# Kernel optimization log

Measured on AMD Instinct MI355X. Metric: run time of the kernel, lower is better.

The kernel has to match this reference:

```python
import jax, jax.numpy as jnp
import numpy as np

EMB_DIM = 256
NUM_HEADS = 4
HEAD_DIM = EMB_DIM // NUM_HEADS
N_EDGES = 320000
N_NODES = 10000
EPS = 1e-16  # torch_geometric softmax epsilon


def setup_inputs() -> dict:
    key = jax.random.key(0)
    kq, kk, ki, kw1, kb1, kw2 = jax.random.split(key, 6)
    q = jax.random.normal(kq, (N_EDGES, EMB_DIM), dtype=jnp.float32)
    k = jax.random.normal(kk, (N_EDGES, EMB_DIM), dtype=jnp.float32)
    index = jnp.sort(jax.random.randint(ki, (N_EDGES,), 0, N_NODES, dtype=jnp.int32))
    # xavier_uniform with gain 1/sqrt(2)
    lim1 = (1.0 / np.sqrt(2.0)) * np.sqrt(6.0 / (2 * EMB_DIM + EMB_DIM))
    w1_w = jax.random.uniform(kw1, (EMB_DIM, 2 * EMB_DIM), dtype=jnp.float32, minval=-lim1, maxval=lim1)
    w1_b = jnp.zeros((EMB_DIM,), dtype=jnp.float32)
    lim2 = (1.0 / np.sqrt(2.0)) * np.sqrt(6.0 / (NUM_HEADS + HEAD_DIM))
    w2 = jax.random.uniform(kw2, (NUM_HEADS, HEAD_DIM), dtype=jnp.float32, minval=-lim2, maxval=lim2)
    return {"q": q, "k": k, "w1_w": w1_w, "w1_b": w1_b, "w2": w2,
            "index": index, "dim_size": N_NODES}


def _segment_softmax(src, index, num_segments):
    # src: [E, H, 1]; index: [E] segment ids; stable softmax per segment per head
    seg_max = jax.ops.segment_max(src, index, num_segments=num_segments)  # [N, H, 1]
    out = jnp.exp(src - seg_max[index])
    seg_sum = jax.ops.segment_sum(out, index, num_segments=num_segments)  # [N, H, 1]
    return out / (seg_sum[index] + EPS)


def reference(q, k, w1_w, w1_b, w2, index, dim_size):
    x = jnp.concatenate([q, k], axis=1)                      # [E, 2D]
    x = x @ w1_w.T + w1_b                                    # [E, D]
    x = jax.nn.leaky_relu(x, negative_slope=0.01)
    x = x.reshape(-1, NUM_HEADS, HEAD_DIM)                   # [E, H, C]
    attn = jnp.einsum('nhc,hc->nh', x, w2)[..., None]        # [E, H, 1]
    return _segment_softmax(attn, index, dim_size)
```

## Files before the change

kernel.cpp:

```cpp
#include <hip/hip_runtime.h>
#include <hip/hip_bf16.h>


typedef __attribute__((ext_vector_type(8))) short bf16x8;
typedef __attribute__((ext_vector_type(4))) float f32x4;
typedef __attribute__((ext_vector_type(4))) short s16x4;

#define NNODES 10000

__device__ __forceinline__ short f2bf(float f) {
    __hip_bfloat16 h = __float2bfloat16(f);
    return *reinterpret_cast<short*>(&h);
}

__device__ __forceinline__ void gload_lds16(const void* g, void* l) {
    __builtin_amdgcn_global_load_lds(
        (const __attribute__((address_space(1))) unsigned int*)g,
        (__attribute__((address_space(3))) unsigned int*)l, 16, 0, 0);
}

__global__ void w1_cvt(const float* __restrict__ w1, short* __restrict__ w1b) {
    int i = (blockIdx.x * 256 + threadIdx.x) * 4;
    float4 v = *(const float4*)(w1 + i);
    s16x4 o; o[0] = f2bf(v.x); o[1] = f2bf(v.y); o[2] = f2bf(v.z); o[3] = f2bf(v.w);
    *(s16x4*)(w1b + i) = o;
}

__global__ void seg_init(float* __restrict__ segsum, int n) {
    int i = blockIdx.x * blockDim.x + threadIdx.x;
    if (i < n) segsum[i] = 0.f;
}

__global__ __launch_bounds__(512, 4) void attn_gemm(
    const float* __restrict__ q, const float* __restrict__ kk_,
    const short* __restrict__ w1b, const float* __restrict__ b1,
    const float* __restrict__ w2, const int* __restrict__ index,
    float* __restrict__ attn, float* __restrict__ segsum)
{
    __shared__ short lds_a[2][128 * 32];
    __shared__ short lds_b[2][256 * 32];

    const int tid  = threadIdx.x;
    const int lane = tid & 63;
    const int w    = tid >> 6;
    const int wm   = w >> 2;
    const int wn   = w & 3;
    const int l15  = lane & 15;
    const int lhi  = lane >> 4;
    const int row0 = blockIdx.x * 128;

    const int b_d    = w * 16 + (lane >> 2);
    const int b_csrc = (lane & 3) ^ ((lane >> 3) & 3);
    const size_t b_off0 = (size_t)b_d * 512 + b_csrc * 8;
    const size_t b_off1 = (size_t)(128 + b_d) * 512 + b_csrc * 8;
    const int b_dst0 = w * 1024 + lane * 16;
    const int b_dst1 = (8 + w) * 1024 + lane * 16;

    const int a_r = tid >> 2;
    const int a_c = tid & 3;
    const size_t a_goff = (size_t)(row0 + a_r) * 256 + a_c * 8;
    const int a_ldst = a_r * 32 + ((a_c ^ ((a_r >> 1) & 3)) * 8);

    f32x4 acc[4][4];
#pragma unroll
    for (int i = 0; i < 4; ++i)
#pragma unroll
        for (int j = 0; j < 4; ++j) acc[i][j] = (f32x4){0.f, 0.f, 0.f, 0.f};

    {
        gload_lds16(w1b + b_off0, (char*)&lds_b[0][0] + b_dst0);
        gload_lds16(w1b + b_off1, (char*)&lds_b[0][0] + b_dst1);
        float4 f0 = *(const float4*)(q + a_goff);
        float4 f1 = *(const float4*)(q + a_goff + 4);
        bf16x8 pk;
        pk[0] = f2bf(f0.x); pk[1] = f2bf(f0.y); pk[2] = f2bf(f0.z); pk[3] = f2bf(f0.w);
        pk[4] = f2bf(f1.x); pk[5] = f2bf(f1.y); pk[6] = f2bf(f1.z); pk[7] = f2bf(f1.w);
        *(bf16x8*)&lds_a[0][a_ldst] = pk;
    }
    __syncthreads();

#pragma unroll
    for (int kt = 0; kt < 16; ++kt) {
        const int cur = kt & 1, nxt = cur ^ 1;

        float4 f0, f1;
        if (kt < 15) {
            const float* abase = (kt + 1 < 8) ? q : kk_;
            const int koff = ((kt + 1) & 7) * 32;
            f0 = *(const float4*)(abase + a_goff + koff);
            f1 = *(const float4*)(abase + a_goff + koff + 4);
            gload_lds16(w1b + b_off0 + (size_t)(kt + 1) * 32, (char*)&lds_b[nxt][0] + b_dst0);
            gload_lds16(w1b + b_off1 + (size_t)(kt + 1) * 32, (char*)&lds_b[nxt][0] + b_dst1);
        }

        bf16x8 af[4], bfv[4];
#pragma unroll
        for (int fm = 0; fm < 4; ++fm) {
            const int r = wm * 64 + fm * 16 + l15;
            af[fm] = *(const bf16x8*)&lds_a[cur][r * 32 + ((lhi ^ ((r >> 1) & 3)) * 8)];
        }
#pragma unroll
        for (int fn = 0; fn < 4; ++fn) {
            const int d = wn * 64 + fn * 16 + l15;
            bfv[fn] = *(const bf16x8*)&lds_b[cur][d * 32 + ((lhi ^ ((d >> 1) & 3)) * 8)];
        }
#pragma unroll
        for (int fm = 0; fm < 4; ++fm)
#pragma unroll
            for (int fn = 0; fn < 4; ++fn)
                acc[fm][fn] = __builtin_amdgcn_mfma_f32_16x16x32_bf16(
                    af[fm], bfv[fn], acc[fm][fn], 0, 0, 0);

        if (kt < 15) {
            bf16x8 pk;
            pk[0] = f2bf(f0.x); pk[1] = f2bf(f0.y); pk[2] = f2bf(f0.z); pk[3] = f2bf(f0.w);
            pk[4] = f2bf(f1.x); pk[5] = f2bf(f1.y); pk[6] = f2bf(f1.z); pk[7] = f2bf(f1.w);
            *(bf16x8*)&lds_a[nxt][a_ldst] = pk;
        }
        __syncthreads();
    }

    float bias[4], w2v[4];
#pragma unroll
    for (int fn = 0; fn < 4; ++fn) {
        int col = wn * 64 + fn * 16 + l15;
        bias[fn] = b1[col];
        w2v[fn]  = w2[col];
    }
#pragma unroll
    for (int fm = 0; fm < 4; ++fm) {
#pragma unroll
        for (int r = 0; r < 4; ++r) {
            int row = row0 + wm * 64 + fm * 16 + lhi * 4 + r;
            float p = 0.f;
#pragma unroll
            for (int fn = 0; fn < 4; ++fn) {
                float y = acc[fm][fn][r] + bias[fn];
                y = (y > 0.f) ? y : 0.01f * y;
                p += y * w2v[fn];
            }
#pragma unroll
            for (int m = 1; m < 16; m <<= 1) p += __shfl_xor(p, m);
            if (l15 == 0) {
                float e = __expf(p);
                attn[(size_t)row * 4 + wn] = e;
                atomicAdd(&segsum[index[row] * 4 + wn], e);
            }
        }
    }
}

__global__ void seg_norm(const float* __restrict__ attn, const int* __restrict__ index,
                         const float* __restrict__ segsum, float* __restrict__ out, int total) {
    int i = blockIdx.x * blockDim.x + threadIdx.x;
    if (i >= total) return;
    int e = i >> 2, h = i & 3;
    out[i] = attn[i] / (segsum[index[e] * 4 + h] + 1e-16f);
}

extern "C" void kernel_launch(void* const* d_in, const int* in_sizes, int n_in,
                              void* d_out, int out_size, void* d_ws, size_t ws_size,
                              hipStream_t stream) {
    const float* q   = (const float*)d_in[0];
    const float* k   = (const float*)d_in[1];
    const float* w1  = (const float*)d_in[2];
    const float* b1  = (const float*)d_in[3];
    const float* w2  = (const float*)d_in[4];
    const int* index = (const int*)d_in[5];

    const int nE = in_sizes[0] / 256;
    char* ws = (char*)d_ws;
    float* attn   = (float*)ws;            ws += (size_t)nE * 4 * 4;
    float* segsum = (float*)ws;            ws += (size_t)NNODES * 4 * 4;
    short* w1bf   = (short*)ws;
    float* out    = (float*)d_out;

    w1_cvt<<<128, 256, 0, stream>>>(w1, w1bf);
    seg_init<<<(NNODES * 4 + 255) / 256, 256, 0, stream>>>(segsum, NNODES * 4);

    attn_gemm<<<nE / 128, 512, 0, stream>>>(q, k, w1bf, b1, w2, index, attn, segsum);

    int total = nE * 4;
    seg_norm<<<(total + 255) / 256, 256, 0, stream>>>(attn, index, segsum, out, total);
}
```

Baseline: 230.0 us.

## Deepen A-operand prefetch to two stages with explicit waitcnt scheduling

Restructures the GEMM main loop so fp32 A-tile global loads are issued two K-steps ahead into a register double buffer, while the B tile is still fetched one step ahead via direct-to-LDS loads. It uses sched_barrier and hand-placed s_waitcnt vmcnt/lgkmcnt counts in place of compiler-chosen waits and __syncthreads. The aim is to hide global load latency behind the MFMAs. In exchange it uses more registers under the 512x4 launch bounds and relies on the exact count of outstanding loads, which is fragile if the compiler reorders or splits the memory ops.

```diff
diff --git a/kernel.cpp b/kernel.cpp
--- a/kernel.cpp
+++ b/kernel.cpp
@@ -67,58 +67,90 @@
 #pragma unroll
         for (int j = 0; j < 4; ++j) acc[i][j] = (f32x4){0.f, 0.f, 0.f, 0.f};
 
-    {
-        gload_lds16(w1b + b_off0, (char*)&lds_b[0][0] + b_dst0);
-        gload_lds16(w1b + b_off1, (char*)&lds_b[0][0] + b_dst1);
-        float4 f0 = *(const float4*)(q + a_goff);
-        float4 f1 = *(const float4*)(q + a_goff + 4);
-        bf16x8 pk;
-        pk[0] = f2bf(f0.x); pk[1] = f2bf(f0.y); pk[2] = f2bf(f0.z); pk[3] = f2bf(f0.w);
-        pk[4] = f2bf(f1.x); pk[5] = f2bf(f1.y); pk[6] = f2bf(f1.z); pk[7] = f2bf(f1.w);
-        *(bf16x8*)&lds_a[0][a_ldst] = pk;
-    }
-    __syncthreads();
-
-#pragma unroll
-    for (int kt = 0; kt < 16; ++kt) {
-        const int cur = kt & 1, nxt = cur ^ 1;
-
-        float4 f0, f1;
-        if (kt < 15) {
-            const float* abase = (kt + 1 < 8) ? q : kk_;
-            const int koff = ((kt + 1) & 7) * 32;
-            f0 = *(const float4*)(abase + a_goff + koff);
-            f1 = *(const float4*)(abase + a_goff + koff + 4);
-            gload_lds16(w1b + b_off0 + (size_t)(kt + 1) * 32, (char*)&lds_b[nxt][0] + b_dst0);
-            gload_lds16(w1b + b_off1 + (size_t)(kt + 1) * 32, (char*)&lds_b[nxt][0] + b_dst1);
-        }
-
-        bf16x8 af[4], bfv[4];
-#pragma unroll
-        for (int fm = 0; fm < 4; ++fm) {
-            const int r = wm * 64 + fm * 16 + l15;
-            af[fm] = *(const bf16x8*)&lds_a[cur][r * 32 + ((lhi ^ ((r >> 1) & 3)) * 8)];
-        }
-#pragma unroll
-        for (int fn = 0; fn < 4; ++fn) {
-            const int d = wn * 64 + fn * 16 + l15;
-            bfv[fn] = *(const bf16x8*)&lds_b[cur][d * 32 + ((lhi ^ ((d >> 1) & 3)) * 8)];
-        }
-#pragma unroll
-        for (int fm = 0; fm < 4; ++fm)
-#pragma unroll
-            for (int fn = 0; fn < 4; ++fn)
-                acc[fm][fn] = __builtin_amdgcn_mfma_f32_16x16x32_bf16(
-                    af[fm], bfv[fn], acc[fm][fn], 0, 0, 0);
-
-        if (kt < 15) {
-            bf16x8 pk;
-            pk[0] = f2bf(f0.x); pk[1] = f2bf(f0.y); pk[2] = f2bf(f0.z); pk[3] = f2bf(f0.w);
-            pk[4] = f2bf(f1.x); pk[5] = f2bf(f1.y); pk[6] = f2bf(f1.z); pk[7] = f2bf(f1.w);
-            *(bf16x8*)&lds_a[nxt][a_ldst] = pk;
-        }
-        __syncthreads();
-    }
+    float4 ra0[2], ra1[2];
+
+#define ISSUE_B(j) {                                                            \
+        gload_lds16(w1b + b_off0 + (size_t)(j) * 32,                            \
+                    (char*)&lds_b[(j) & 1][0] + b_dst0);                        \
+        gload_lds16(w1b + b_off1 + (size_t)(j) * 32,                            \
+                    (char*)&lds_b[(j) & 1][0] + b_dst1);                        \
+    }
+#define LOAD_A(j) {                                                             \
+        const float* ab = ((j) < 8) ? q : kk_;                                  \
+        const float* p  = ab + a_goff + (((j) & 7) * 32);                       \
+        ra0[(j) & 1] = *(const float4*)p;                                       \
+        ra1[(j) & 1] = *(const float4*)(p + 4);                                 \
+    }
+#define WRITE_A(j) {                                                            \
+        bf16x8 pk;                                                              \
+        pk[0] = f2bf(ra0[(j) & 1].x); pk[1] = f2bf(ra0[(j) & 1].y);             \
+        pk[2] = f2bf(ra0[(j) & 1].z); pk[3] = f2bf(ra0[(j) & 1].w);             \
+        pk[4] = f2bf(ra1[(j) & 1].x); pk[5] = f2bf(ra1[(j) & 1].y);             \
+        pk[6] = f2bf(ra1[(j) & 1].z); pk[7] = f2bf(ra1[(j) & 1].w);             \
+        *(bf16x8*)&lds_a[(j) & 1][a_ldst] = pk;                                 \
+    }
+#define FRAG_MFMA(cur) {                                                        \
+        bf16x8 af[4], bfv[4];                                                   \
+        _Pragma("unroll")                                                       \
+        for (int fm = 0; fm < 4; ++fm) {                                        \
+            const int r = wm * 64 + fm * 16 + l15;                              \
+            af[fm] = *(const bf16x8*)&lds_a[cur][r * 32 + ((lhi ^ ((r >> 1) & 3)) * 8)]; \
+        }                                                                       \
+        _Pragma("unroll")                                                       \
+        for (int fn = 0; fn < 4; ++fn) {                                        \
+            const int d = wn * 64 + fn * 16 + l15;                              \
+            bfv[fn] = *(const bf16x8*)&lds_b[cur][d * 32 + ((lhi ^ ((d >> 1) & 3)) * 8)]; \
+        }                                                                       \
+        _Pragma("unroll")                                                       \
+        for (int fm = 0; fm < 4; ++fm)                                          \
+            _Pragma("unroll")                                                   \
+            for (int fn = 0; fn < 4; ++fn)                                      \
+                acc[fm][fn] = __builtin_amdgcn_mfma_f32_16x16x32_bf16(          \
+                    af[fm], bfv[fn], acc[fm][fn], 0, 0, 0);                     \
+    }
+
+    ISSUE_B(0);
+    __builtin_amdgcn_sched_barrier(0);
+    LOAD_A(0);
+    __builtin_amdgcn_sched_barrier(0);
+    LOAD_A(1);
+    __builtin_amdgcn_sched_barrier(0);
+    asm volatile("s_waitcnt vmcnt(2)" ::: "memory");
+    WRITE_A(0);
+    asm volatile("s_waitcnt lgkmcnt(0)" ::: "memory");
+    __builtin_amdgcn_s_barrier();
+    __builtin_amdgcn_sched_barrier(0);
+
+#pragma unroll
+    for (int kt = 0; kt < 14; ++kt) {
+        const int cur = kt & 1;
+        ISSUE_B(kt + 1);
+        __builtin_amdgcn_sched_barrier(0);
+        LOAD_A(kt + 2);
+        __builtin_amdgcn_sched_barrier(0);
+        FRAG_MFMA(cur);
+        asm volatile("s_waitcnt vmcnt(4)" ::: "memory");
+        WRITE_A(kt + 1);
+        asm volatile("s_waitcnt vmcnt(2) lgkmcnt(0)" ::: "memory");
+        __builtin_amdgcn_s_barrier();
+        __builtin_amdgcn_sched_barrier(0);
+    }
+
+    ISSUE_B(15);
+    __builtin_amdgcn_sched_barrier(0);
+    FRAG_MFMA(0);
+    asm volatile("s_waitcnt vmcnt(2)" ::: "memory");
+    WRITE_A(15);
+    asm volatile("s_waitcnt vmcnt(0) lgkmcnt(0)" ::: "memory");
+    __builtin_amdgcn_s_barrier();
+    __builtin_amdgcn_sched_barrier(0);
+
+    FRAG_MFMA(1);
+
+#undef ISSUE_B
+#undef LOAD_A
+#undef WRITE_A
+#undef FRAG_MFMA
 
     float bias[4], w2v[4];
 #pragma unroll
```

Result: slower. 245.9 us (+6.9%).

## Enlarge GEMM tile to 256 rows with deeper K-step and prefetch pipeline

Applied to the files above, without the earlier changes.

Rows per block grow from 128 to 256 and each K step from 32 to 64. The kernel now uses 128 KB of dynamic LDS with an XOR swizzle, and register prefetch of A is staged two steps ahead. The MFMA phases are split with explicit waitcnt, barriers and setprio so global loads, bf16 conversion and matrix ops interleave. This should raise reuse of W1 per block and hide memory latency. In exchange, occupancy drops to about one block per CU, register pressure rises, and the hand-placed wait counts must be exactly right.

```diff
diff --git a/kernel.cpp b/kernel.cpp
--- a/kernel.cpp
+++ b/kernel.cpp
@@ -31,14 +31,13 @@
     if (i < n) segsum[i] = 0.f;
 }
 
-__global__ __launch_bounds__(512, 4) void attn_gemm(
+__global__ __launch_bounds__(512, 2) void attn_gemm(
     const float* __restrict__ q, const float* __restrict__ kk_,
     const short* __restrict__ w1b, const float* __restrict__ b1,
     const float* __restrict__ w2, const int* __restrict__ index,
     float* __restrict__ attn, float* __restrict__ segsum)
 {
-    __shared__ short lds_a[2][128 * 32];
-    __shared__ short lds_b[2][256 * 32];
+    extern __shared__ __align__(16) short smem[];
 
     const int tid  = threadIdx.x;
     const int lane = tid & 63;
@@ -47,77 +46,119 @@
     const int wn   = w & 3;
     const int l15  = lane & 15;
     const int lhi  = lane >> 4;
-    const int row0 = blockIdx.x * 128;
-
-    const int b_d    = w * 16 + (lane >> 2);
-    const int b_csrc = (lane & 3) ^ ((lane >> 3) & 3);
-    const size_t b_off0 = (size_t)b_d * 512 + b_csrc * 8;
-    const size_t b_off1 = (size_t)(128 + b_d) * 512 + b_csrc * 8;
-    const int b_dst0 = w * 1024 + lane * 16;
-    const int b_dst1 = (8 + w) * 1024 + lane * 16;
-
-    const int a_r = tid >> 2;
-    const int a_c = tid & 3;
-    const size_t a_goff = (size_t)(row0 + a_r) * 256 + a_c * 8;
-    const int a_ldst = a_r * 32 + ((a_c ^ ((a_r >> 1) & 3)) * 8);
-
-    f32x4 acc[4][4];
-#pragma unroll
-    for (int i = 0; i < 4; ++i)
+    const int row0 = blockIdx.x * 256;
+
+    const int arow = tid >> 3;
+    const int asub = tid & 7;
+    const int xsub = asub ^ (arow & 7);
+    const int aw0  = arow * 128 + xsub * 16;
+
+    f32x4 acc[8][4];
+#pragma unroll
+    for (int i = 0; i < 8; ++i)
 #pragma unroll
         for (int j = 0; j < 4; ++j) acc[i][j] = (f32x4){0.f, 0.f, 0.f, 0.f};
 
+    float4 ar0[4], ar1[4];
+
     {
-        gload_lds16(w1b + b_off0, (char*)&lds_b[0][0] + b_dst0);
-        gload_lds16(w1b + b_off1, (char*)&lds_b[0][0] + b_dst1);
-        float4 f0 = *(const float4*)(q + a_goff);
-        float4 f1 = *(const float4*)(q + a_goff + 4);
-        bf16x8 pk;
-        pk[0] = f2bf(f0.x); pk[1] = f2bf(f0.y); pk[2] = f2bf(f0.z); pk[3] = f2bf(f0.w);
-        pk[4] = f2bf(f1.x); pk[5] = f2bf(f1.y); pk[6] = f2bf(f1.z); pk[7] = f2bf(f1.w);
-        *(bf16x8*)&lds_a[0][a_ldst] = pk;
-    }
-    __syncthreads();
-
-#pragma unroll
-    for (int kt = 0; kt < 16; ++kt) {
-        const int cur = kt & 1, nxt = cur ^ 1;
-
-        float4 f0, f1;
-        if (kt < 15) {
-            const float* abase = (kt + 1 < 8) ? q : kk_;
-            const int koff = ((kt + 1) & 7) * 32;
-            f0 = *(const float4*)(abase + a_goff + koff);
-            f1 = *(const float4*)(abase + a_goff + koff + 4);
-            gload_lds16(w1b + b_off0 + (size_t)(kt + 1) * 32, (char*)&lds_b[nxt][0] + b_dst0);
-            gload_lds16(w1b + b_off1 + (size_t)(kt + 1) * 32, (char*)&lds_b[nxt][0] + b_dst1);
-        }
-
-        bf16x8 af[4], bfv[4];
-#pragma unroll
-        for (int fm = 0; fm < 4; ++fm) {
-            const int r = wm * 64 + fm * 16 + l15;
-            af[fm] = *(const bf16x8*)&lds_a[cur][r * 32 + ((lhi ^ ((r >> 1) & 3)) * 8)];
-        }
-#pragma unroll
-        for (int fn = 0; fn < 4; ++fn) {
-            const int d = wn * 64 + fn * 16 + l15;
-            bfv[fn] = *(const bf16x8*)&lds_b[cur][d * 32 + ((lhi ^ ((d >> 1) & 3)) * 8)];
-        }
-#pragma unroll
-        for (int fm = 0; fm < 4; ++fm)
-#pragma unroll
-            for (int fn = 0; fn < 4; ++fn)
-                acc[fm][fn] = __builtin_amdgcn_mfma_f32_16x16x32_bf16(
-                    af[fm], bfv[fn], acc[fm][fn], 0, 0, 0);
-
-        if (kt < 15) {
+#pragma unroll
+        for (int c = 0; c < 4; ++c) {
+            const float* p = q + (size_t)(row0 + c * 64 + arow) * 256 + asub * 8;
+            ar0[c] = *(const float4*)p; ar1[c] = *(const float4*)(p + 4);
+        }
+        char* bb = (char*)(smem + 32768);
+#pragma unroll
+        for (int i2 = 0; i2 < 4; ++i2)
+            gload_lds16(w1b + i2 * 32768 + arow * 512 + xsub * 8,
+                        bb + (i2 * 512 + tid) * 16);
+        asm volatile("s_waitcnt vmcnt(4)" ::: "memory");
+        __builtin_amdgcn_sched_barrier(0);
+        char* dA = (char*)smem;
+#pragma unroll
+        for (int c = 0; c < 4; ++c) {
             bf16x8 pk;
-            pk[0] = f2bf(f0.x); pk[1] = f2bf(f0.y); pk[2] = f2bf(f0.z); pk[3] = f2bf(f0.w);
-            pk[4] = f2bf(f1.x); pk[5] = f2bf(f1.y); pk[6] = f2bf(f1.z); pk[7] = f2bf(f1.w);
-            *(bf16x8*)&lds_a[nxt][a_ldst] = pk;
-        }
-        __syncthreads();
+            pk[0] = f2bf(ar0[c].x); pk[1] = f2bf(ar0[c].y);
+            pk[2] = f2bf(ar0[c].z); pk[3] = f2bf(ar0[c].w);
+            pk[4] = f2bf(ar1[c].x); pk[5] = f2bf(ar1[c].y);
+            pk[6] = f2bf(ar1[c].z); pk[7] = f2bf(ar1[c].w);
+            *(bf16x8*)(dA + c * 8192 + aw0) = pk;
+            const float* p = q + (size_t)(row0 + c * 64 + arow) * 256 + 64 + asub * 8;
+            ar0[c] = *(const float4*)p; ar1[c] = *(const float4*)(p + 4);
+        }
+        asm volatile("s_waitcnt vmcnt(8)" ::: "memory");
+        __builtin_amdgcn_sched_barrier(0);
+        asm volatile("s_waitcnt lgkmcnt(0)" ::: "memory");
+        __builtin_amdgcn_s_barrier();
+    }
+
+    bf16x8 bfr[4];
+#pragma unroll 2
+    for (int g = 0; g < 8; ++g) {
+        const int cur = g & 1, nxt = cur ^ 1;
+        const int SM1 = (g + 1) & 7;
+        const int SM2 = (g + 2) & 7;
+        const int koB = SM1 * 64;
+        const float* a2b = (SM2 < 4) ? q : kk_;
+        const int koA = (SM2 & 3) * 64;
+        const char* sA = (const char*)(smem + cur * 16384);
+        const char* sB = (const char*)(smem + 32768 + cur * 16384);
+        char* dA = (char*)(smem + nxt * 16384);
+        char* dB = (char*)(smem + 32768 + nxt * 16384);
+#pragma unroll
+        for (int p = 0; p < 4; ++p) {
+            const int kk = p >> 1;
+            const int fb = (p & 1) * 4;
+            if ((p & 1) == 0) {
+#pragma unroll
+                for (int fn = 0; fn < 4; ++fn) {
+                    const int d = wn * 64 + fn * 16 + l15;
+                    bfr[fn] = *(const bf16x8*)(sB + d * 128 +
+                               ((kk * 64 + lhi * 16) ^ ((d & 7) << 4)));
+                }
+            }
+            bf16x8 afr[4];
+#pragma unroll
+            for (int i2 = 0; i2 < 4; ++i2) {
+                const int r = wm * 128 + (fb + i2) * 16 + l15;
+                afr[i2] = *(const bf16x8*)(sA + r * 128 +
+                           ((kk * 64 + lhi * 16) ^ ((r & 7) << 4)));
+            }
+            if (p == 0) {
+#pragma unroll
+                for (int i2 = 0; i2 < 4; ++i2)
+                    gload_lds16(w1b + i2 * 32768 + arow * 512 + xsub * 8 + koB,
+                                dB + (i2 * 512 + tid) * 16);
+            }
+            asm volatile("s_waitcnt vmcnt(10)" ::: "memory");
+            __builtin_amdgcn_sched_barrier(0);
+            {
+                bf16x8 pk;
+                pk[0] = f2bf(ar0[p].x); pk[1] = f2bf(ar0[p].y);
+                pk[2] = f2bf(ar0[p].z); pk[3] = f2bf(ar0[p].w);
+                pk[4] = f2bf(ar1[p].x); pk[5] = f2bf(ar1[p].y);
+                pk[6] = f2bf(ar1[p].z); pk[7] = f2bf(ar1[p].w);
+                *(bf16x8*)(dA + p * 8192 + aw0) = pk;
+                const float* pp = a2b + (size_t)(row0 + p * 64 + arow) * 256 + koA + asub * 8;
+                ar0[p] = *(const float4*)pp; ar1[p] = *(const float4*)(pp + 4);
+            }
+            if (p == 3) {
+                asm volatile("s_waitcnt vmcnt(8)" ::: "memory");
+                __builtin_amdgcn_sched_barrier(0);
+            }
+            __builtin_amdgcn_s_barrier();
+            asm volatile("s_waitcnt lgkmcnt(0)" ::: "memory");
+            __builtin_amdgcn_sched_barrier(0);
+            __builtin_amdgcn_s_setprio(1);
+#pragma unroll
+            for (int i2 = 0; i2 < 4; ++i2)
+#pragma unroll
+                for (int fn = 0; fn < 4; ++fn)
+                    acc[fb + i2][fn] = __builtin_amdgcn_mfma_f32_16x16x32_bf16(
+                        afr[i2], bfr[fn], acc[fb + i2][fn], 0, 0, 0);
+            __builtin_amdgcn_s_setprio(0);
+            __builtin_amdgcn_s_barrier();
+        }
     }
 
     float bias[4], w2v[4];
@@ -128,10 +169,10 @@
         w2v[fn]  = w2[col];
     }
 #pragma unroll
-    for (int fm = 0; fm < 4; ++fm) {
+    for (int fm = 0; fm < 8; ++fm) {
 #pragma unroll
         for (int r = 0; r < 4; ++r) {
-            int row = row0 + wm * 64 + fm * 16 + lhi * 4 + r;
+            int row = row0 + wm * 128 + fm * 16 + lhi * 4 + r;
             float p = 0.f;
 #pragma unroll
             for (int fn = 0; fn < 4; ++fn) {
@@ -175,10 +216,13 @@
     short* w1bf   = (short*)ws;
     float* out    = (float*)d_out;
 
+    hipFuncSetAttribute((const void*)attn_gemm,
+                        hipFuncAttributeMaxDynamicSharedMemorySize, 131072);
+
     w1_cvt<<<128, 256, 0, stream>>>(w1, w1bf);
     seg_init<<<(NNODES * 4 + 255) / 256, 256, 0, stream>>>(segsum, NNODES * 4);
 
-    attn_gemm<<<nE / 128, 512, 0, stream>>>(q, k, w1bf, b1, w2, index, attn, segsum);
+    attn_gemm<<<nE / 256, 512, 131072, stream>>>(q, k, w1bf, b1, w2, index, attn, segsum);
 
     int total = nE * 4;
     seg_norm<<<(total + 255) / 256, 256, 0, stream>>>(attn, index, segsum, out, total);
```

Measured after the change: 249.0 us. +8.3%, slower.

## Load W1 as pre-swizzled MFMA fragments from global and process two tiles per block

Applied to the files above, without the earlier changes.

W1 is pre-converted into an MFMA fragment-ordered bf16 layout so each wave reads its B fragments directly from global (L2-resident) instead of staging them through LDS. The A tile now uses 64-wide K steps with an XOR swizzle, a register prefetch pipeline that spans tile boundaries, and a lighter barrier. Each block handles two 128-row tiles to amortize setup and keep the pipeline full. The gains come from freeing LDS and removing B-staging traffic, at the cost of more global/L2 load pressure and a grid size hard-coded to the edge count.

```diff
diff --git a/kernel.cpp b/kernel.cpp
--- a/kernel.cpp
+++ b/kernel.cpp
@@ -4,26 +4,29 @@
 
 typedef __attribute__((ext_vector_type(8))) short bf16x8;
 typedef __attribute__((ext_vector_type(4))) float f32x4;
-typedef __attribute__((ext_vector_type(4))) short s16x4;
 
 #define NNODES 10000
+#define NT     2500
+#define TPB    2
+#define GRID   (NT / TPB)
 
 __device__ __forceinline__ short f2bf(float f) {
     __hip_bfloat16 h = __float2bfloat16(f);
     return *reinterpret_cast<short*>(&h);
 }
 
-__device__ __forceinline__ void gload_lds16(const void* g, void* l) {
-    __builtin_amdgcn_global_load_lds(
-        (const __attribute__((address_space(1))) unsigned int*)g,
-        (__attribute__((address_space(3))) unsigned int*)l, 16, 0, 0);
-}
-
-__global__ void w1_cvt(const float* __restrict__ w1, short* __restrict__ w1b) {
-    int i = (blockIdx.x * 256 + threadIdx.x) * 4;
-    float4 v = *(const float4*)(w1 + i);
-    s16x4 o; o[0] = f2bf(v.x); o[1] = f2bf(v.y); o[2] = f2bf(v.z); o[3] = f2bf(v.w);
-    *(s16x4*)(w1b + i) = o;
+__global__ void w1_frag(const float* __restrict__ w1, short* __restrict__ wf) {
+    int bid = blockIdx.x;
+    int l   = threadIdx.x;
+    int n = (bid >> 4) * 16 + (l & 15);
+    int k = (bid & 15) * 32 + (l >> 4) * 8;
+    const float* src = w1 + (size_t)n * 512 + k;
+    float4 v0 = *(const float4*)src;
+    float4 v1 = *(const float4*)(src + 4);
+    bf16x8 pk;
+    pk[0]=f2bf(v0.x); pk[1]=f2bf(v0.y); pk[2]=f2bf(v0.z); pk[3]=f2bf(v0.w);
+    pk[4]=f2bf(v1.x); pk[5]=f2bf(v1.y); pk[6]=f2bf(v1.z); pk[7]=f2bf(v1.w);
+    *(bf16x8*)(wf + ((size_t)bid * 64 + l) * 8) = pk;
 }
 
 __global__ void seg_init(float* __restrict__ segsum, int n) {
@@ -33,12 +36,11 @@
 
 __global__ __launch_bounds__(512, 4) void attn_gemm(
     const float* __restrict__ q, const float* __restrict__ kk_,
-    const short* __restrict__ w1b, const float* __restrict__ b1,
+    const short* __restrict__ wf, const float* __restrict__ b1,
     const float* __restrict__ w2, const int* __restrict__ index,
     float* __restrict__ attn, float* __restrict__ segsum)
 {
-    __shared__ short lds_a[2][128 * 32];
-    __shared__ short lds_b[2][256 * 32];
+    __shared__ short lds_a[2][128 * 64];
 
     const int tid  = threadIdx.x;
     const int lane = tid & 63;
@@ -47,78 +49,15 @@
     const int wn   = w & 3;
     const int l15  = lane & 15;
     const int lhi  = lane >> 4;
-    const int row0 = blockIdx.x * 128;
-
-    const int b_d    = w * 16 + (lane >> 2);
-    const int b_csrc = (lane & 3) ^ ((lane >> 3) & 3);
-    const size_t b_off0 = (size_t)b_d * 512 + b_csrc * 8;
-    const size_t b_off1 = (size_t)(128 + b_d) * 512 + b_csrc * 8;
-    const int b_dst0 = w * 1024 + lane * 16;
-    const int b_dst1 = (8 + w) * 1024 + lane * 16;
-
-    const int a_r = tid >> 2;
-    const int a_c = tid & 3;
-    const size_t a_goff = (size_t)(row0 + a_r) * 256 + a_c * 8;
-    const int a_ldst = a_r * 32 + ((a_c ^ ((a_r >> 1) & 3)) * 8);
+
+    const int rt  = tid >> 2;
+    const int kcg = (tid & 3) * 2;
+    const int wbyte0 = rt * 128 + ((((kcg + 0) * 16)) ^ ((rt & 7) << 4));
+    const int wbyte1 = rt * 128 + ((((kcg + 1) * 16)) ^ ((rt & 7) << 4));
+
+    float4 ar[4];
 
     f32x4 acc[4][4];
-#pragma unroll
-    for (int i = 0; i < 4; ++i)
-#pragma unroll
-        for (int j = 0; j < 4; ++j) acc[i][j] = (f32x4){0.f, 0.f, 0.f, 0.f};
-
-    {
-        gload_lds16(w1b + b_off0, (char*)&lds_b[0][0] + b_dst0);
-        gload_lds16(w1b + b_off1, (char*)&lds_b[0][0] + b_dst1);
-        float4 f0 = *(const float4*)(q + a_goff);
-        float4 f1 = *(const float4*)(q + a_goff + 4);
-        bf16x8 pk;
-        pk[0] = f2bf(f0.x); pk[1] = f2bf(f0.y); pk[2] = f2bf(f0.z); pk[3] = f2bf(f0.w);
-        pk[4] = f2bf(f1.x); pk[5] = f2bf(f1.y); pk[6] = f2bf(f1.z); pk[7] = f2bf(f1.w);
-        *(bf16x8*)&lds_a[0][a_ldst] = pk;
-    }
-    __syncthreads();
-
-#pragma unroll
-    for (int kt = 0; kt < 16; ++kt) {
-        const int cur = kt & 1, nxt = cur ^ 1;
-
-        float4 f0, f1;
-        if (kt < 15) {
-            const float* abase = (kt + 1 < 8) ? q : kk_;
-            const int koff = ((kt + 1) & 7) * 32;
-            f0 = *(const float4*)(abase + a_goff + koff);
-            f1 = *(const float4*)(abase + a_goff + koff + 4);
-            gload_lds16(w1b + b_off0 + (size_t)(kt + 1) * 32, (char*)&lds_b[nxt][0] + b_dst0);
-            gload_lds16(w1b + b_off1 + (size_t)(kt + 1) * 32, (char*)&lds_b[nxt][0] + b_dst1);
-        }
-
-        bf16x8 af[4], bfv[4];
-#pragma unroll
-        for (int fm = 0; fm < 4; ++fm) {
-            const int r = wm * 64 + fm * 16 + l15;
-            af[fm] = *(const bf16x8*)&lds_a[cur][r * 32 + ((lhi ^ ((r >> 1) & 3)) * 8)];
-        }
-#pragma unroll
-        for (int fn = 0; fn < 4; ++fn) {
-            const int d = wn * 64 + fn * 16 + l15;
-            bfv[fn] = *(const bf16x8*)&lds_b[cur][d * 32 + ((lhi ^ ((d >> 1) & 3)) * 8)];
-        }
-#pragma unroll
-        for (int fm = 0; fm < 4; ++fm)
-#pragma unroll
-            for (int fn = 0; fn < 4; ++fn)
-                acc[fm][fn] = __builtin_amdgcn_mfma_f32_16x16x32_bf16(
-                    af[fm], bfv[fn], acc[fm][fn], 0, 0, 0);
-
-        if (kt < 15) {
-            bf16x8 pk;
-            pk[0] = f2bf(f0.x); pk[1] = f2bf(f0.y); pk[2] = f2bf(f0.z); pk[3] = f2bf(f0.w);
-            pk[4] = f2bf(f1.x); pk[5] = f2bf(f1.y); pk[6] = f2bf(f1.z); pk[7] = f2bf(f1.w);
-            *(bf16x8*)&lds_a[nxt][a_ldst] = pk;
-        }
-        __syncthreads();
-    }
 
     float bias[4], w2v[4];
 #pragma unroll
@@ -127,27 +66,104 @@
         bias[fn] = b1[col];
         w2v[fn]  = w2[col];
     }
-#pragma unroll
-    for (int fm = 0; fm < 4; ++fm) {
-#pragma unroll
-        for (int r = 0; r < 4; ++r) {
-            int row = row0 + wm * 64 + fm * 16 + lhi * 4 + r;
-            float p = 0.f;
-#pragma unroll
-            for (int fn = 0; fn < 4; ++fn) {
-                float y = acc[fm][fn][r] + bias[fn];
-                y = (y > 0.f) ? y : 0.01f * y;
-                p += y * w2v[fn];
-            }
-#pragma unroll
-            for (int m = 1; m < 16; m <<= 1) p += __shfl_xor(p, m);
-            if (l15 == 0) {
-                float e = __expf(p);
-                attn[(size_t)row * 4 + wn] = e;
-                atomicAdd(&segsum[index[row] * 4 + wn], e);
+
+#define LOADA(T, S) {                                                           \
+        const float* bp = ((S) < 4) ? q : kk_;                                  \
+        const float* p  = bp + (size_t)((T) * 128 + rt) * 256                   \
+                             + ((S) & 3) * 64 + (tid & 3) * 16;                 \
+        ar[0] = *(const float4*)p;      ar[1] = *(const float4*)(p + 4);        \
+        ar[2] = *(const float4*)(p + 8); ar[3] = *(const float4*)(p + 12);      \
+    }
+#define CVTWRITE(wb) {                                                          \
+        bf16x8 p0, p1;                                                          \
+        p0[0]=f2bf(ar[0].x); p0[1]=f2bf(ar[0].y); p0[2]=f2bf(ar[0].z); p0[3]=f2bf(ar[0].w); \
+        p0[4]=f2bf(ar[1].x); p0[5]=f2bf(ar[1].y); p0[6]=f2bf(ar[1].z); p0[7]=f2bf(ar[1].w); \
+        p1[0]=f2bf(ar[2].x); p1[1]=f2bf(ar[2].y); p1[2]=f2bf(ar[2].z); p1[3]=f2bf(ar[2].w); \
+        p1[4]=f2bf(ar[3].x); p1[5]=f2bf(ar[3].y); p1[6]=f2bf(ar[3].z); p1[7]=f2bf(ar[3].w); \
+        *(bf16x8*)((char*)&lds_a[wb][0] + wbyte0) = p0;                         \
+        *(bf16x8*)((char*)&lds_a[wb][0] + wbyte1) = p1;                         \
+    }
+#define FRAGMFMA(rb, s) {                                                       \
+        _Pragma("unroll")                                                       \
+        for (int ks = 0; ks < 2; ++ks) {                                        \
+            bf16x8 bfr[4], afr[4];                                              \
+            _Pragma("unroll")                                                   \
+            for (int fn = 0; fn < 4; ++fn)                                      \
+                bfr[fn] = *(const bf16x8*)(wf +                                 \
+                    (((size_t)((wn * 4 + fn) * 16 + (s) * 2 + ks) * 64 + lane) * 8)); \
+            _Pragma("unroll")                                                   \
+            for (int fm = 0; fm < 4; ++fm) {                                    \
+                const int r = wm * 64 + fm * 16 + l15;                          \
+                afr[fm] = *(const bf16x8*)((const char*)&lds_a[rb][0]           \
+                    + r * 128 + ((((ks * 4 + lhi) * 16)) ^ ((r & 7) << 4)));    \
+            }                                                                   \
+            _Pragma("unroll")                                                   \
+            for (int fm = 0; fm < 4; ++fm)                                      \
+                _Pragma("unroll")                                               \
+                for (int fn = 0; fn < 4; ++fn)                                  \
+                    acc[fm][fn] = __builtin_amdgcn_mfma_f32_16x16x32_bf16(      \
+                        afr[fm], bfr[fn], acc[fm][fn], 0, 0, 0);                \
+        }                                                                       \
+    }
+#define BAR() {                                                                 \
+        asm volatile("s_waitcnt lgkmcnt(0)" ::: "memory");                      \
+        __builtin_amdgcn_s_barrier();                                           \
+    }
+
+    const int tile0 = blockIdx.x * TPB;
+
+    LOADA(tile0, 0);
+    CVTWRITE(0);
+    LOADA(tile0, 1);
+    BAR();
+
+#pragma unroll
+    for (int ti = 0; ti < TPB; ++ti) {
+        const int tile  = tile0 + ti;
+        const int tnext = tile0 + ((ti + 1 < TPB) ? ti + 1 : ti);
+
+#pragma unroll
+        for (int i = 0; i < 4; ++i)
+#pragma unroll
+            for (int j = 0; j < 4; ++j) acc[i][j] = (f32x4){0.f, 0.f, 0.f, 0.f};
+
+#pragma unroll
+        for (int s = 0; s < 8; ++s) {
+            const int rb = s & 1, wb = rb ^ 1;
+            CVTWRITE(wb);
+            if (s < 6) { LOADA(tile, s + 2); }
+            else       { LOADA(tnext, s - 6); }
+            FRAGMFMA(rb, s);
+            BAR();
+        }
+
+#pragma unroll
+        for (int fm = 0; fm < 4; ++fm) {
+#pragma unroll
+            for (int r = 0; r < 4; ++r) {
+                int row = tile * 128 + wm * 64 + fm * 16 + lhi * 4 + r;
+                float p = 0.f;
+#pragma unroll
+                for (int fn = 0; fn < 4; ++fn) {
+                    float y = acc[fm][fn][r] + bias[fn];
+                    y = (y > 0.f) ? y : 0.01f * y;
+                    p += y * w2v[fn];
+                }
+#pragma unroll
+                for (int m = 1; m < 16; m <<= 1) p += __shfl_xor(p, m);
+                if (l15 == 0) {
+                    float e = __expf(p);
+                    attn[(size_t)row * 4 + wn] = e;
+                    atomicAdd(&segsum[index[row] * 4 + wn], e);
+                }
             }
         }
     }
+
+#undef LOADA
+#undef CVTWRITE
+#undef FRAGMFMA
+#undef BAR
 }
 
 __global__ void seg_norm(const float* __restrict__ attn, const int* __restrict__ index,
@@ -172,13 +188,13 @@
     char* ws = (char*)d_ws;
     float* attn   = (float*)ws;            ws += (size_t)nE * 4 * 4;
     float* segsum = (float*)ws;            ws += (size_t)NNODES * 4 * 4;
-    short* w1bf   = (short*)ws;
+    short* wf     = (short*)ws;
     float* out    = (float*)d_out;
 
-    w1_cvt<<<128, 256, 0, stream>>>(w1, w1bf);
+    w1_frag<<<256, 64, 0, stream>>>(w1, wf);
     seg_init<<<(NNODES * 4 + 255) / 256, 256, 0, stream>>>(segsum, NNODES * 4);
 
-    attn_gemm<<<nE / 128, 512, 0, stream>>>(q, k, w1bf, b1, w2, index, attn, segsum);
+    attn_gemm<<<GRID, 512, 0, stream>>>(q, k, wf, b1, w2, index, attn, segsum);
 
     int total = nE * 4;
     seg_norm<<<(total + 255) / 256, 256, 0, stream>>>(attn, index, segsum, out, total);
```

New measurement: 365.1 us. 1.59x slower.
